# Kernel tuning notes

Hardware: AMD Instinct MI355X
Metric: run time of the kernel (lower is better)

Reference implementation:

```python
import jax, jax.numpy as jnp
import numpy as np

C_QKV = 128
C_HID = 32
N_HEADS = 4
INF = 1e9


def setup_inputs() -> dict:
    key = jax.random.key(0)
    ks = jax.random.split(key, 8)
    B, S = 256, 256
    hc = N_HEADS * C_HID  # 128
    inp = {
        "input_qkv": jax.random.normal(ks[0], (1, B, S, C_QKV), dtype=jnp.float32),
        "mask": jnp.ones((1, B, 1, 1, S), dtype=jnp.float32),
        "bias": jax.random.normal(ks[1], (1, 1, N_HEADS, S, S), dtype=jnp.float32),
        "add_transposed_output_to": jax.random.normal(ks[2], (1, B, S, C_QKV), dtype=jnp.float32),
        # linear_qkvg: Linear(c_qkv, 4*h*c), bias=False -> weight [4*hc, c_qkv]
        "W_qkvg": jax.random.normal(ks[3], (4 * hc, C_QKV), dtype=jnp.float32) * (1.0 / np.sqrt(C_QKV)),
        # gating bias initialized to ones in the module
        "linear_g_bias": jnp.ones((hc,), dtype=jnp.float32),
        # linear_o: Linear(hc, c_qkv), init='final' (zeros in AF2, use small random for a nontrivial test)
        "W_o": jax.random.normal(ks[4], (C_QKV, hc), dtype=jnp.float32) * (1.0 / np.sqrt(hc)),
        "b_o": jax.random.normal(ks[5], (C_QKV,), dtype=jnp.float32) * 0.02,
    }
    return inp


def reference(input_qkv, mask, bias, add_transposed_output_to, W_qkvg, linear_g_bias, W_o, b_o):
    hc = N_HEADS * C_HID
    # fused QKVG projection: [1, b, s, 4*hc]
    qkvg = jnp.einsum("xbsc,fc->xbsf", input_qkv, W_qkvg)
    q, k, v, g = jnp.split(qkvg, 4, axis=-1)
    # reshape to heads: [1, b, s, h, c]
    shp = q.shape[:-1] + (N_HEADS, C_HID)
    q = q.reshape(shp)
    k = k.reshape(shp)
    v = v.reshape(shp)
    scale = 1.0 / np.sqrt(C_HID)
    # scores: [1, b, h, q, k]
    a = jnp.einsum("xbqhc,xbkhc->xbhqk", q * scale, k)
    a = a + (mask - 1.0) * INF + bias
    a = jax.nn.softmax(a, axis=-1)
    # attention output: [1, b, q, h, c] -> [1, b, s, hc]
    o = jnp.einsum("xbhqk,xbkhc->xbqhc", a, v)
    o = o.reshape(o.shape[:-2] + (hc,))
    # sigmoid gating
    o = o * jax.nn.sigmoid(g + linear_g_bias)
    # fused linear + transpose(-2,-3) + add
    proj = jnp.einsum("xbsf,of->xbso", o, W_o) + b_o  # [1, b, s, c_qkv]
    out = add_transposed_output_to + jnp.swapaxes(proj, -2, -3)  # [1, s, b, c_qkv]
    return out
```

## Files before the change

### kernel.cpp

```cpp
#include <hip/hip_runtime.h>
#include <math.h>

#define BB 256
#define SS 256
#define NH 4

typedef __attribute__((ext_vector_type(8))) short bfrag;
typedef __attribute__((ext_vector_type(4))) float ffrag;

__device__ inline unsigned short f2bf(float x) {
    unsigned u = __float_as_uint(x);
    u += 0x7FFF + ((u >> 16) & 1);
    return (unsigned short)(u >> 16);
}
__device__ inline float bf2f(unsigned short h) {
    return __uint_as_float(((unsigned)h) << 16);
}
__device__ inline unsigned pack2(float a, float b) {
    return (unsigned)f2bf(a) | ((unsigned)f2bf(b) << 16);
}
union FragU { unsigned u[4]; bfrag b; };

#define XB_OFF  0
#define WB_OFF  8388608
#define WOB_OFF 8454144
#define OG_OFF  8470528

__global__ __launch_bounds__(256) void k0_cast(
    const float* __restrict__ X, const float* __restrict__ W,
    const float* __restrict__ Wo, unsigned short* __restrict__ dst)
{
    const int gid = blockIdx.x * 256 + threadIdx.x;
    const int XN8 = 8388608 / 8, WN8 = 65536 / 8, WoN8 = 16384 / 8;
    const float* src;
    size_t soff, doff;
    if (gid < XN8)            { src = X;  soff = (size_t)gid * 8;                 doff = XB_OFF + soff; }
    else if (gid < XN8 + WN8) { src = W;  soff = (size_t)(gid - XN8) * 8;         doff = WB_OFF + soff; }
    else if (gid < XN8 + WN8 + WoN8) { src = Wo; soff = (size_t)(gid - XN8 - WN8) * 8; doff = WOB_OFF + soff; }
    else return;
    const float4 a = *(const float4*)(src + soff);
    const float4 b = *(const float4*)(src + soff + 4);
    unsigned r0 = pack2(a.x, a.y), r1 = pack2(a.z, a.w);
    unsigned r2 = pack2(b.x, b.y), r3 = pack2(b.z, b.w);
    uint4 o; o.x = r0; o.y = r1; o.z = r2; o.w = r3;
    *(uint4*)(dst + doff) = o;
}

__global__ __launch_bounds__(256, 2) void k_fused(
    const unsigned short* __restrict__ Xb,
    const unsigned short* __restrict__ Wb,
    const float* __restrict__ gbias,
    const float* __restrict__ mask,
    const float* __restrict__ bias,
    unsigned short* __restrict__ og)
{
    const int h = blockIdx.x, b = blockIdx.y;
    const int t = threadIdx.x;
    const int w = t >> 6, lane = t & 63, l15 = lane & 15, quad = lane >> 4;

    __shared__ unsigned short Kb[SS * 40];
    __shared__ unsigned short Vt[32 * 264];
    __shared__ float maskLds[SS];

    maskLds[t] = (mask[b * SS + t] - 1.0f) * 1e9f;

    const float qscale = 0.17677669529663687f;

    FragU qa0, qa1, qa2, qa3;
    unsigned g0c0a, g0c0b, g0c1a, g0c1b;
    unsigned g1c0a, g1c0b, g1c1a, g1c1b;
    unsigned g2c0a, g2c0b, g2c1a, g2c1b;
    unsigned g3c0a, g3c0b, g3c1a, g3c1b;

#pragma unroll
    for (int half = 0; half < 2; ++half) {
        bfrag Wfr[4][4];
#pragma unroll
        for (int f4 = 0; f4 < 4; ++f4) {
            const int floc = (half * 4 + f4) * 16 + l15;
            const int grow = (floc >> 5) * 128 + h * 32 + (floc & 31);
#pragma unroll
            for (int cc = 0; cc < 4; ++cc)
                Wfr[f4][cc] = *(const bfrag*)(Wb + grow * 128 + cc * 32 + quad * 8);
        }
#pragma unroll
        for (int st = 0; st < 4; ++st) {
            const int s = w * 64 + st * 16 + l15;
            bfrag Xfr[4];
#pragma unroll
            for (int cc = 0; cc < 4; ++cc)
                Xfr[cc] = *(const bfrag*)(Xb + (b * SS + s) * 128 + cc * 32 + quad * 8);
#pragma unroll
            for (int f4 = 0; f4 < 4; ++f4) {
                const int ft = half * 4 + f4;
                if (ft < 2) {
                    ffrag D = {0.f, 0.f, 0.f, 0.f};
#pragma unroll
                    for (int cc = 0; cc < 4; ++cc)
                        D = __builtin_amdgcn_mfma_f32_16x16x32_bf16(Wfr[f4][cc], Xfr[cc], D, 0, 0, 0);
                    const unsigned lo = pack2(D[0] * qscale, D[1] * qscale);
                    const unsigned hi = pack2(D[2] * qscale, D[3] * qscale);
                    FragU* qa = (st == 0) ? &qa0 : (st == 1) ? &qa1 : (st == 2) ? &qa2 : &qa3;
                    if (ft == 0) { qa->u[0] = lo; qa->u[1] = hi; }
                    else         { qa->u[2] = lo; qa->u[3] = hi; }
                } else if (ft < 4) {
                    ffrag D = {0.f, 0.f, 0.f, 0.f};
#pragma unroll
                    for (int cc = 0; cc < 4; ++cc)
                        D = __builtin_amdgcn_mfma_f32_16x16x32_bf16(Xfr[cc], Wfr[f4][cc], D, 0, 0, 0);
                    const int c = (ft - 2) * 16 + l15;
                    const int p = ((c & 15) >> 2) * 8 + (c & 3) + ((c >> 4) << 2);
                    const int srow0 = w * 64 + st * 16 + quad * 4;
#pragma unroll
                    for (int r = 0; r < 4; ++r)
                        Kb[(srow0 + r) * 40 + p] = f2bf(D[r]);
                } else if (ft < 6) {
                    ffrag D = {0.f, 0.f, 0.f, 0.f};
#pragma unroll
                    for (int cc = 0; cc < 4; ++cc)
                        D = __builtin_amdgcn_mfma_f32_16x16x32_bf16(Xfr[cc], Wfr[f4][cc], D, 0, 0, 0);
                    const int fcol = ft * 16 + l15;
                    const int srow0 = w * 64 + st * 16 + quad * 4;
                    const int base = (fcol - 64) * 264 + srow0;
                    *(unsigned*)&Vt[base]     = pack2(D[0], D[1]);
                    *(unsigned*)&Vt[base + 2] = pack2(D[2], D[3]);
                } else {
                    ffrag D = {0.f, 0.f, 0.f, 0.f};
#pragma unroll
                    for (int cc = 0; cc < 4; ++cc)
                        D = __builtin_amdgcn_mfma_f32_16x16x32_bf16(Wfr[f4][cc], Xfr[cc], D, 0, 0, 0);
                    const int ch = ft - 6;
                    float gv[4];
#pragma unroll
                    for (int r = 0; r < 4; ++r) {
                        const float gb = gbias[h * 32 + ch * 16 + quad * 4 + r];
                        gv[r] = 1.0f / (1.0f + __expf(-(D[r] + gb)));
                    }
                    const unsigned pa = pack2(gv[0], gv[1]);
                    const unsigned pb = pack2(gv[2], gv[3]);
                    if (st == 0) { if (ch == 0) { g0c0a = pa; g0c0b = pb; } else { g0c1a = pa; g0c1b = pb; } }
                    if (st == 1) { if (ch == 0) { g1c0a = pa; g1c0b = pb; } else { g1c1a = pa; g1c1b = pb; } }
                    if (st == 2) { if (ch == 0) { g2c0a = pa; g2c0b = pb; } else { g2c1a = pa; g2c1b = pb; } }
                    if (st == 3) { if (ch == 0) { g3c0a = pa; g3c0b = pb; } else { g3c1a = pa; g3c1b = pb; } }
                }
            }
        }
    }
    __syncthreads();

    const int srcA = l15 + ((quad & 1) * 2) * 16;
    const int srcB = srcA + 16;
    const bool hi = (quad >> 1) != 0;

    for (int qq = 0; qq < 4; ++qq) {
        const int q = w * 64 + qq * 16 + l15;
        bfrag Qfr;
        unsigned gc0a, gc0b, gc1a, gc1b;
        if (qq == 0)      { Qfr = qa0.b; gc0a = g0c0a; gc0b = g0c0b; gc1a = g0c1a; gc1b = g0c1b; }
        else if (qq == 1) { Qfr = qa1.b; gc0a = g1c0a; gc0b = g1c0b; gc1a = g1c1a; gc1b = g1c1b; }
        else if (qq == 2) { Qfr = qa2.b; gc0a = g2c0a; gc0b = g2c0b; gc1a = g2c1a; gc1b = g2c1b; }
        else              { Qfr = qa3.b; gc0a = g3c0a; gc0b = g3c0b; gc1a = g3c1a; gc1b = g3c1b; }

        ffrag S[16];
#pragma unroll
        for (int kt = 0; kt < 16; ++kt) {
            const bfrag Kfr = *(const bfrag*)&Kb[(kt * 16 + l15) * 40 + quad * 8];
            const ffrag z = {0.f, 0.f, 0.f, 0.f};
            S[kt] = __builtin_amdgcn_mfma_f32_16x16x32_bf16(Kfr, Qfr, z, 0, 0, 0);
        }

        const float* brow = bias + (h * SS + q) * SS;
        float m = -1e30f;
#pragma unroll
        for (int kt = 0; kt < 16; ++kt) {
            const float4 bv = *(const float4*)(brow + kt * 16 + quad * 4);
            const float4 mv = *(const float4*)(maskLds + kt * 16 + quad * 4);
            S[kt][0] += bv.x + mv.x; S[kt][1] += bv.y + mv.y;
            S[kt][2] += bv.z + mv.z; S[kt][3] += bv.w + mv.w;
            m = fmaxf(m, fmaxf(fmaxf(S[kt][0], S[kt][1]), fmaxf(S[kt][2], S[kt][3])));
        }
        m = fmaxf(m, __shfl_xor(m, 16, 64));
        m = fmaxf(m, __shfl_xor(m, 32, 64));

        float l = 0.f;
        unsigned pk[16][2];
#pragma unroll
        for (int kt = 0; kt < 16; ++kt) {
            const float p0 = __expf(S[kt][0] - m);
            const float p1 = __expf(S[kt][1] - m);
            const float p2 = __expf(S[kt][2] - m);
            const float p3 = __expf(S[kt][3] - m);
            l += (p0 + p1) + (p2 + p3);
            pk[kt][0] = pack2(p0, p1);
            pk[kt][1] = pack2(p2, p3);
        }
        l += __shfl_xor(l, 16, 64);
        l += __shfl_xor(l, 32, 64);

        ffrag O[2];
        O[0] = (ffrag){0.f, 0.f, 0.f, 0.f};
        O[1] = (ffrag){0.f, 0.f, 0.f, 0.f};
#pragma unroll
        for (int ck = 0; ck < 8; ++ck) {
            const unsigned a0 = (unsigned)__shfl((int)pk[2 * ck][0],     srcA, 64);
            const unsigned b0 = (unsigned)__shfl((int)pk[2 * ck + 1][0], srcA, 64);
            const unsigned a1 = (unsigned)__shfl((int)pk[2 * ck][1],     srcA, 64);
            const unsigned b1 = (unsigned)__shfl((int)pk[2 * ck + 1][1], srcA, 64);
            const unsigned a2 = (unsigned)__shfl((int)pk[2 * ck][0],     srcB, 64);
            const unsigned b2 = (unsigned)__shfl((int)pk[2 * ck + 1][0], srcB, 64);
            const unsigned a3 = (unsigned)__shfl((int)pk[2 * ck][1],     srcB, 64);
            const unsigned b3 = (unsigned)__shfl((int)pk[2 * ck + 1][1], srcB, 64);
            FragU fu;
            fu.u[0] = hi ? b0 : a0;
            fu.u[1] = hi ? b1 : a1;
            fu.u[2] = hi ? b2 : a2;
            fu.u[3] = hi ? b3 : a3;
            const bfrag v0 = *(const bfrag*)&Vt[(l15) * 264 + ck * 32 + quad * 8];
            const bfrag v1 = *(const bfrag*)&Vt[(16 + l15) * 264 + ck * 32 + quad * 8];
            O[0] = __builtin_amdgcn_mfma_f32_16x16x32_bf16(v0, fu.b, O[0], 0, 0, 0);
            O[1] = __builtin_amdgcn_mfma_f32_16x16x32_bf16(v1, fu.b, O[1], 0, 0, 0);
        }

        const float invl = 1.0f / l;
        unsigned* orow = (unsigned*)(og + (b * SS + q) * 128 + h * 32);
#pragma unroll
        for (int ch = 0; ch < 2; ++ch) {
            const unsigned ga = ch ? gc1a : gc0a;
            const unsigned gb2 = ch ? gc1b : gc0b;
            const int c0 = ch * 16 + quad * 4;
            const float v0 = O[ch][0] * invl * bf2f((unsigned short)(ga & 0xffff));
            const float v1 = O[ch][1] * invl * bf2f((unsigned short)(ga >> 16));
            const float v2 = O[ch][2] * invl * bf2f((unsigned short)(gb2 & 0xffff));
            const float v3 = O[ch][3] * invl * bf2f((unsigned short)(gb2 >> 16));
            orow[(c0 >> 1) + 0] = pack2(v0, v1);
            orow[(c0 >> 1) + 1] = pack2(v2, v3);
        }
    }
}

__global__ __launch_bounds__(256) void k3_proj(
    const unsigned short* __restrict__ ogb,
    const unsigned short* __restrict__ Wob,
    const float* __restrict__ bo,
    const float* __restrict__ addt,
    float* __restrict__ out)
{
    const int j = blockIdx.x, ih = blockIdx.y;
    const int t = threadIdx.x;
    const int w = t >> 6, lane = t & 63, l15 = lane & 15, quad = lane >> 4;

    __shared__ unsigned short OgS[64 * 136];
    __shared__ float OutS[64 * 132];

    {
        const int ss = t >> 2;
        const int c32 = (t & 3) * 32;
        const unsigned short* src = ogb + (((size_t)j * SS + ih * 64 + ss) * 128) + c32;
        unsigned short* dst = &OgS[ss * 136 + c32];
#pragma unroll
        for (int u = 0; u < 4; ++u)
            *(uint4*)(dst + u * 8) = *(const uint4*)(src + u * 8);
    }

    bfrag Wfr[2][4];
#pragma unroll
    for (int ctl = 0; ctl < 2; ++ctl) {
        const int crow = (w * 2 + ctl) * 16 + l15;
#pragma unroll
        for (int cc = 0; cc < 4; ++cc)
            Wfr[ctl][cc] = *(const bfrag*)(Wob + crow * 128 + cc * 32 + quad * 8);
    }
    const float bo0 = bo[(w * 2 + 0) * 16 + l15];
    const float bo1 = bo[(w * 2 + 1) * 16 + l15];

    __syncthreads();

#pragma unroll
    for (int jt = 0; jt < 4; ++jt) {
        bfrag Ab[4];
#pragma unroll
        for (int cc = 0; cc < 4; ++cc)
            Ab[cc] = *(const bfrag*)&OgS[(jt * 16 + l15) * 136 + cc * 32 + quad * 8];

        ffrag D0 = {0.f, 0.f, 0.f, 0.f};
        ffrag D1 = {0.f, 0.f, 0.f, 0.f};
#pragma unroll
        for (int cc = 0; cc < 4; ++cc) {
            D0 = __builtin_amdgcn_mfma_f32_16x16x32_bf16(Ab[cc], Wfr[0][cc], D0, 0, 0, 0);
            D1 = __builtin_amdgcn_mfma_f32_16x16x32_bf16(Ab[cc], Wfr[1][cc], D1, 0, 0, 0);
        }

        const int c0 = (w * 2 + 0) * 16 + l15;
        const int c1 = (w * 2 + 1) * 16 + l15;
#pragma unroll
        for (int r = 0; r < 4; ++r) {
            const int row = jt * 16 + quad * 4 + r;
            OutS[row * 132 + c0] = D0[r] + bo0;
            OutS[row * 132 + c1] = D1[r] + bo1;
        }
    }
    __syncthreads();

    {
        const int c4 = lane & 31;
        const int rsub = t >> 5;
#pragma unroll
        for (int v = 0; v < 8; ++v) {
            const int row = v * 8 + rsub;
            const int s = ih * 64 + row;
            const size_t off = ((size_t)s * BB + j) * 128 + c4 * 4;
            const float4 av = *(const float4*)(addt + off);
            const float4 dv = *(const float4*)&OutS[row * 132 + c4 * 4];
            float4 ov;
            ov.x = dv.x + av.x; ov.y = dv.y + av.y;
            ov.z = dv.z + av.z; ov.w = dv.w + av.w;
            *(float4*)(out + off) = ov;
        }
    }
}

extern "C" void kernel_launch(void* const* d_in, const int* in_sizes, int n_in,
                              void* d_out, int out_size, void* d_ws, size_t ws_size,
                              hipStream_t stream) {
    const float* X     = (const float*)d_in[0];
    const float* mask  = (const float*)d_in[1];
    const float* bias  = (const float*)d_in[2];
    const float* addt  = (const float*)d_in[3];
    const float* Wqkvg = (const float*)d_in[4];
    const float* gbias = (const float*)d_in[5];
    const float* Wo    = (const float*)d_in[6];
    const float* bo    = (const float*)d_in[7];
    float* out = (float*)d_out;

    unsigned short* ws = (unsigned short*)d_ws;
    unsigned short* Xb  = ws + XB_OFF;
    unsigned short* Wb  = ws + WB_OFF;
    unsigned short* Wob = ws + WOB_OFF;
    unsigned short* og  = ws + OG_OFF;

    k0_cast<<<4136, 256, 0, stream>>>(X, Wqkvg, Wo, ws);
    k_fused<<<dim3(NH, BB), 256, 0, stream>>>(Xb, Wb, gbias, mask, bias, og);
    k3_proj<<<dim3(BB, 4), 256, 0, stream>>>(og, Wob, bo, addt, out);
}
```

Measured before the change: 257.4 us.

## Use online softmax over key chunks and stream W fragments to cut registers

The attention loop now processes keys in four chunks with an online (running max and rescale) softmax instead of holding all 16 score tiles and packed probabilities in registers. The QKVG projection loop is reordered so only one W fragment set (4 fragments) is live at a time, with X fragments reloaded per feature tile. Both changes aim to lower VGPR pressure and so raise occupancy. The cost is extra exp and rescale work per chunk and more X loads.

```diff
diff --git a/kernel.cpp b/kernel.cpp
--- a/kernel.cpp
+++ b/kernel.cpp
@@ -74,30 +74,27 @@
 
 #pragma unroll
     for (int half = 0; half < 2; ++half) {
-        bfrag Wfr[4][4];
 #pragma unroll
         for (int f4 = 0; f4 < 4; ++f4) {
-            const int floc = (half * 4 + f4) * 16 + l15;
+            const int ft = half * 4 + f4;
+            const int floc = ft * 16 + l15;
             const int grow = (floc >> 5) * 128 + h * 32 + (floc & 31);
+            bfrag Wfr[4];
 #pragma unroll
             for (int cc = 0; cc < 4; ++cc)
-                Wfr[f4][cc] = *(const bfrag*)(Wb + grow * 128 + cc * 32 + quad * 8);
-        }
-#pragma unroll
-        for (int st = 0; st < 4; ++st) {
-            const int s = w * 64 + st * 16 + l15;
-            bfrag Xfr[4];
-#pragma unroll
-            for (int cc = 0; cc < 4; ++cc)
-                Xfr[cc] = *(const bfrag*)(Xb + (b * SS + s) * 128 + cc * 32 + quad * 8);
-#pragma unroll
-            for (int f4 = 0; f4 < 4; ++f4) {
-                const int ft = half * 4 + f4;
+                Wfr[cc] = *(const bfrag*)(Wb + grow * 128 + cc * 32 + quad * 8);
+#pragma unroll
+            for (int st = 0; st < 4; ++st) {
+                const int s = w * 64 + st * 16 + l15;
+                bfrag Xfr[4];
+#pragma unroll
+                for (int cc = 0; cc < 4; ++cc)
+                    Xfr[cc] = *(const bfrag*)(Xb + (b * SS + s) * 128 + cc * 32 + quad * 8);
                 if (ft < 2) {
                     ffrag D = {0.f, 0.f, 0.f, 0.f};
 #pragma unroll
                     for (int cc = 0; cc < 4; ++cc)
-                        D = __builtin_amdgcn_mfma_f32_16x16x32_bf16(Wfr[f4][cc], Xfr[cc], D, 0, 0, 0);
+                        D = __builtin_amdgcn_mfma_f32_16x16x32_bf16(Wfr[cc], Xfr[cc], D, 0, 0, 0);
                     const unsigned lo = pack2(D[0] * qscale, D[1] * qscale);
                     const unsigned hi = pack2(D[2] * qscale, D[3] * qscale);
                     FragU* qa = (st == 0) ? &qa0 : (st == 1) ? &qa1 : (st == 2) ? &qa2 : &qa3;
@@ -107,7 +104,7 @@
                     ffrag D = {0.f, 0.f, 0.f, 0.f};
 #pragma unroll
                     for (int cc = 0; cc < 4; ++cc)
-                        D = __builtin_amdgcn_mfma_f32_16x16x32_bf16(Xfr[cc], Wfr[f4][cc], D, 0, 0, 0);
+                        D = __builtin_amdgcn_mfma_f32_16x16x32_bf16(Xfr[cc], Wfr[cc], D, 0, 0, 0);
                     const int c = (ft - 2) * 16 + l15;
                     const int p = ((c & 15) >> 2) * 8 + (c & 3) + ((c >> 4) << 2);
                     const int srow0 = w * 64 + st * 16 + quad * 4;
@@ -118,7 +115,7 @@
                     ffrag D = {0.f, 0.f, 0.f, 0.f};
 #pragma unroll
                     for (int cc = 0; cc < 4; ++cc)
-                        D = __builtin_amdgcn_mfma_f32_16x16x32_bf16(Xfr[cc], Wfr[f4][cc], D, 0, 0, 0);
+                        D = __builtin_amdgcn_mfma_f32_16x16x32_bf16(Xfr[cc], Wfr[cc], D, 0, 0, 0);
                     const int fcol = ft * 16 + l15;
                     const int srow0 = w * 64 + st * 16 + quad * 4;
                     const int base = (fcol - 64) * 264 + srow0;
@@ -128,7 +125,7 @@
                     ffrag D = {0.f, 0.f, 0.f, 0.f};
 #pragma unroll
                     for (int cc = 0; cc < 4; ++cc)
-                        D = __builtin_amdgcn_mfma_f32_16x16x32_bf16(Wfr[f4][cc], Xfr[cc], D, 0, 0, 0);
+                        D = __builtin_amdgcn_mfma_f32_16x16x32_bf16(Wfr[cc], Xfr[cc], D, 0, 0, 0);
                     const int ch = ft - 6;
                     float gv[4];
 #pragma unroll
@@ -161,66 +158,78 @@
         else if (qq == 2) { Qfr = qa2.b; gc0a = g2c0a; gc0b = g2c0b; gc1a = g2c1a; gc1b = g2c1b; }
         else              { Qfr = qa3.b; gc0a = g3c0a; gc0b = g3c0b; gc1a = g3c1a; gc1b = g3c1b; }
 
-        ffrag S[16];
-#pragma unroll
-        for (int kt = 0; kt < 16; ++kt) {
-            const bfrag Kfr = *(const bfrag*)&Kb[(kt * 16 + l15) * 40 + quad * 8];
-            const ffrag z = {0.f, 0.f, 0.f, 0.f};
-            S[kt] = __builtin_amdgcn_mfma_f32_16x16x32_bf16(Kfr, Qfr, z, 0, 0, 0);
-        }
-
         const float* brow = bias + (h * SS + q) * SS;
-        float m = -1e30f;
-#pragma unroll
-        for (int kt = 0; kt < 16; ++kt) {
-            const float4 bv = *(const float4*)(brow + kt * 16 + quad * 4);
-            const float4 mv = *(const float4*)(maskLds + kt * 16 + quad * 4);
-            S[kt][0] += bv.x + mv.x; S[kt][1] += bv.y + mv.y;
-            S[kt][2] += bv.z + mv.z; S[kt][3] += bv.w + mv.w;
-            m = fmaxf(m, fmaxf(fmaxf(S[kt][0], S[kt][1]), fmaxf(S[kt][2], S[kt][3])));
-        }
-        m = fmaxf(m, __shfl_xor(m, 16, 64));
-        m = fmaxf(m, __shfl_xor(m, 32, 64));
-
-        float l = 0.f;
-        unsigned pk[16][2];
-#pragma unroll
-        for (int kt = 0; kt < 16; ++kt) {
-            const float p0 = __expf(S[kt][0] - m);
-            const float p1 = __expf(S[kt][1] - m);
-            const float p2 = __expf(S[kt][2] - m);
-            const float p3 = __expf(S[kt][3] - m);
-            l += (p0 + p1) + (p2 + p3);
-            pk[kt][0] = pack2(p0, p1);
-            pk[kt][1] = pack2(p2, p3);
-        }
-        l += __shfl_xor(l, 16, 64);
-        l += __shfl_xor(l, 32, 64);
-
         ffrag O[2];
         O[0] = (ffrag){0.f, 0.f, 0.f, 0.f};
         O[1] = (ffrag){0.f, 0.f, 0.f, 0.f};
-#pragma unroll
-        for (int ck = 0; ck < 8; ++ck) {
-            const unsigned a0 = (unsigned)__shfl((int)pk[2 * ck][0],     srcA, 64);
-            const unsigned b0 = (unsigned)__shfl((int)pk[2 * ck + 1][0], srcA, 64);
-            const unsigned a1 = (unsigned)__shfl((int)pk[2 * ck][1],     srcA, 64);
-            const unsigned b1 = (unsigned)__shfl((int)pk[2 * ck + 1][1], srcA, 64);
-            const unsigned a2 = (unsigned)__shfl((int)pk[2 * ck][0],     srcB, 64);
-            const unsigned b2 = (unsigned)__shfl((int)pk[2 * ck + 1][0], srcB, 64);
-            const unsigned a3 = (unsigned)__shfl((int)pk[2 * ck][1],     srcB, 64);
-            const unsigned b3 = (unsigned)__shfl((int)pk[2 * ck + 1][1], srcB, 64);
-            FragU fu;
-            fu.u[0] = hi ? b0 : a0;
-            fu.u[1] = hi ? b1 : a1;
-            fu.u[2] = hi ? b2 : a2;
-            fu.u[3] = hi ? b3 : a3;
-            const bfrag v0 = *(const bfrag*)&Vt[(l15) * 264 + ck * 32 + quad * 8];
-            const bfrag v1 = *(const bfrag*)&Vt[(16 + l15) * 264 + ck * 32 + quad * 8];
-            O[0] = __builtin_amdgcn_mfma_f32_16x16x32_bf16(v0, fu.b, O[0], 0, 0, 0);
-            O[1] = __builtin_amdgcn_mfma_f32_16x16x32_bf16(v1, fu.b, O[1], 0, 0, 0);
-        }
-
+        float m = -1e30f, l = 0.f;
+
+#pragma unroll
+        for (int c = 0; c < 4; ++c) {
+            ffrag S[4];
+#pragma unroll
+            for (int i = 0; i < 4; ++i) {
+                const int kt = 4 * c + i;
+                const bfrag Kfr = *(const bfrag*)&Kb[(kt * 16 + l15) * 40 + quad * 8];
+                const ffrag z = {0.f, 0.f, 0.f, 0.f};
+                S[i] = __builtin_amdgcn_mfma_f32_16x16x32_bf16(Kfr, Qfr, z, 0, 0, 0);
+            }
+            float cm = -1e30f;
+#pragma unroll
+            for (int i = 0; i < 4; ++i) {
+                const int kt = 4 * c + i;
+                const float4 bv = *(const float4*)(brow + kt * 16 + quad * 4);
+                const float4 mv = *(const float4*)(maskLds + kt * 16 + quad * 4);
+                S[i][0] += bv.x + mv.x; S[i][1] += bv.y + mv.y;
+                S[i][2] += bv.z + mv.z; S[i][3] += bv.w + mv.w;
+                cm = fmaxf(cm, fmaxf(fmaxf(S[i][0], S[i][1]), fmaxf(S[i][2], S[i][3])));
+            }
+            cm = fmaxf(cm, __shfl_xor(cm, 16, 64));
+            cm = fmaxf(cm, __shfl_xor(cm, 32, 64));
+            const float mnew = fmaxf(m, cm);
+            const float scale = __expf(m - mnew);
+            O[0][0] *= scale; O[0][1] *= scale; O[0][2] *= scale; O[0][3] *= scale;
+            O[1][0] *= scale; O[1][1] *= scale; O[1][2] *= scale; O[1][3] *= scale;
+            l *= scale;
+
+            unsigned pk[4][2];
+#pragma unroll
+            for (int i = 0; i < 4; ++i) {
+                const float p0 = __expf(S[i][0] - mnew);
+                const float p1 = __expf(S[i][1] - mnew);
+                const float p2 = __expf(S[i][2] - mnew);
+                const float p3 = __expf(S[i][3] - mnew);
+                l += (p0 + p1) + (p2 + p3);
+                pk[i][0] = pack2(p0, p1);
+                pk[i][1] = pack2(p2, p3);
+            }
+
+#pragma unroll
+            for (int ck2 = 0; ck2 < 2; ++ck2) {
+                const int ck = 2 * c + ck2;
+                const unsigned a0 = (unsigned)__shfl((int)pk[2 * ck2][0],     srcA, 64);
+                const unsigned b0 = (unsigned)__shfl((int)pk[2 * ck2 + 1][0], srcA, 64);
+                const unsigned a1 = (unsigned)__shfl((int)pk[2 * ck2][1],     srcA, 64);
+                const unsigned b1 = (unsigned)__shfl((int)pk[2 * ck2 + 1][1], srcA, 64);
+                const unsigned a2 = (unsigned)__shfl((int)pk[2 * ck2][0],     srcB, 64);
+                const unsigned b2 = (unsigned)__shfl((int)pk[2 * ck2 + 1][0], srcB, 64);
+                const unsigned a3 = (unsigned)__shfl((int)pk[2 * ck2][1],     srcB, 64);
+                const unsigned b3 = (unsigned)__shfl((int)pk[2 * ck2 + 1][1], srcB, 64);
+                FragU fu;
+                fu.u[0] = hi ? b0 : a0;
+                fu.u[1] = hi ? b1 : a1;
+                fu.u[2] = hi ? b2 : a2;
+                fu.u[3] = hi ? b3 : a3;
+                const bfrag v0 = *(const bfrag*)&Vt[(l15) * 264 + ck * 32 + quad * 8];
+                const bfrag v1 = *(const bfrag*)&Vt[(16 + l15) * 264 + ck * 32 + quad * 8];
+                O[0] = __builtin_amdgcn_mfma_f32_16x16x32_bf16(v0, fu.b, O[0], 0, 0, 0);
+                O[1] = __builtin_amdgcn_mfma_f32_16x16x32_bf16(v1, fu.b, O[1], 0, 0, 0);
+            }
+            m = mnew;
+        }
+
+        l += __shfl_xor(l, 16, 64);
+        l += __shfl_xor(l, 32, 64);
         const float invl = 1.0f / l;
         unsigned* orow = (unsigned*)(og + (b * SS + q) * 128 + h * 32);
 #pragma unroll
```

After: 254.5 us. Within noise of the previous version (-1.1%).
